# Optimization experiments

Measured on AMD Instinct MI355X. Metric: run time of the kernel, lower is better.

Reference implementation:

```python
import jax, jax.numpy as jnp
import numpy as np

ALPHA = 0.4
EPS = float(np.finfo(np.float32).eps)  # torch.finfo(fp32).eps
BATCH, VOCAB, RANK = 256, 128000, 64


def setup_inputs() -> dict:
    key = jax.random.key(0)
    k1, k2, k3 = jax.random.split(key, 3)
    token_ids = jax.random.randint(k1, (BATCH, 1), 0, VOCAB, dtype=jnp.int64 if jax.config.jax_enable_x64 else jnp.int32)
    logits = jax.random.normal(k2, (BATCH, VOCAB), dtype=jnp.float32)
    W = jax.random.normal(k3, (VOCAB, RANK), dtype=jnp.float32)
    return {"token_ids": token_ids, "logits": logits, "W": W}


def reference(token_ids, logits, W):
    # _rescaled_mint_no_cast (remove_basis=True):
    #   Lp_raw = L @ W @ W.T - L   (low-rank mint, basis removed)
    Lp_raw = (logits @ W) @ W.T - logits  # [B, V]
    # Guarantee max|L'| <= max|L| via global abs-max rescale.
    scale = jnp.max(jnp.abs(logits)) / jnp.maximum(jnp.max(jnp.abs(Lp_raw)), EPS)
    minted = Lp_raw * scale
    # Modes.Lerp: torch.lerp(minted, logits, alpha) = minted + alpha*(logits - minted)
    return minted + ALPHA * (logits - minted)
```

## Files before the change

kernel.cpp:

```cpp
#include <hip/hip_runtime.h>
#include <math.h>

#define ALPHA_F 0.4f
#define FP32_EPS 1.1920928955078125e-7f
#define NB 256
#define NV 128000
#define NR 64

typedef _Float16 half_t;
typedef _Float16 half2_t __attribute__((ext_vector_type(2)));
typedef _Float16 half8 __attribute__((ext_vector_type(8)));
typedef float f32x4 __attribute__((ext_vector_type(4)));


__global__ __launch_bounds__(256) void k0_prep(const float* __restrict__ W,
                                               half_t* __restrict__ WhT,
                                               float* __restrict__ P,
                                               unsigned* __restrict__ maxbits) {
    __shared__ half_t tile[256 * 66];
    const int t  = threadIdx.x;
    const int k0 = blockIdx.x * 256;

    if (blockIdx.x < 64) P[blockIdx.x * 256 + t] = 0.f;
    if (blockIdx.x == 0 && t < 2) maxbits[t] = 0u;

#pragma unroll
    for (int i = 0; i < 16; ++i) {
        const int f  = i * 256 + t;
        const int kr = f >> 4;
        const int n4 = (f & 15) * 4;
        const float4 v = *(const float4*)(W + (size_t)(k0 + kr) * NR + n4);
        half2_t h01 = { (half_t)v.x, (half_t)v.y };
        half2_t h23 = { (half_t)v.z, (half_t)v.w };
        *(half2_t*)&tile[kr * 66 + n4]     = h01;
        *(half2_t*)&tile[kr * 66 + n4 + 2] = h23;
    }
    __syncthreads();

    const int n   = t >> 2;
    const int seg = t & 3;
#pragma unroll
    for (int i = 0; i < 8; ++i) {
        const int kk = (i * 4 + seg) * 8;
        half8 v;
#pragma unroll
        for (int j = 0; j < 8; ++j) v[j] = tile[(kk + j) * 66 + n];
        *(half8*)(WhT + (size_t)n * NV + k0 + kk) = v;
    }
}

__global__ __launch_bounds__(256) void k1_pmm(const float* __restrict__ L,
                                              const half_t* __restrict__ WhT,
                                              float* __restrict__ Ppart,
                                              unsigned* __restrict__ maxbits) {
    const int l  = threadIdx.x & 63;
    const int w  = threadIdx.x >> 6;
    const int q  = l >> 4;
    const int il = l & 15;
    const int k0 = blockIdx.x * 256;

    f32x4 acc[4][4] = {};
    float amax = 0.f;

    for (int ks = 0; ks < 8; ++ks) {
        const int kk = k0 + ks * 32 + q * 8;
        half8 b[4];
#pragma unroll
        for (int nt = 0; nt < 4; ++nt)
            b[nt] = *(const half8*)(WhT + (size_t)(nt * 16 + il) * NV + kk);
#pragma unroll
        for (int mt = 0; mt < 4; ++mt) {
            const float* lp = L + (size_t)(mt * 64 + w * 16 + il) * NV + kk;
            const float4 f0 = *(const float4*)lp;
            const float4 f1 = *(const float4*)(lp + 4);
            amax = fmaxf(amax, fmaxf(fmaxf(fabsf(f0.x), fabsf(f0.y)),
                                     fmaxf(fabsf(f0.z), fabsf(f0.w))));
            amax = fmaxf(amax, fmaxf(fmaxf(fabsf(f1.x), fabsf(f1.y)),
                                     fmaxf(fabsf(f1.z), fabsf(f1.w))));
            half8 a = { (half_t)f0.x, (half_t)f0.y, (half_t)f0.z, (half_t)f0.w,
                        (half_t)f1.x, (half_t)f1.y, (half_t)f1.z, (half_t)f1.w };
#pragma unroll
            for (int nt = 0; nt < 4; ++nt)
                acc[mt][nt] = __builtin_amdgcn_mfma_f32_16x16x32_f16(a, b[nt], acc[mt][nt], 0, 0, 0);
        }
    }

    float* pb = Ppart + (size_t)blockIdx.x * (NB * NR);
#pragma unroll
    for (int mt = 0; mt < 4; ++mt)
#pragma unroll
        for (int nt = 0; nt < 4; ++nt)
#pragma unroll
            for (int i = 0; i < 4; ++i)
                pb[(mt * 64 + w * 16 + q * 4 + i) * NR + nt * 16 + il] = acc[mt][nt][i];

#pragma unroll
    for (int off = 32; off > 0; off >>= 1)
        amax = fmaxf(amax, __shfl_xor(amax, off, 64));
    __shared__ float red[4];
    if (l == 0) red[w] = amax;
    __syncthreads();
    if (threadIdx.x == 0) {
        float m = fmaxf(fmaxf(red[0], red[1]), fmaxf(red[2], red[3]));
        atomicMax(&maxbits[0], __float_as_uint(m));
    }
}

__global__ __launch_bounds__(256) void k1b_reduce(const float* __restrict__ Ppart,
                                                  float* __restrict__ P) {
    const int g = blockIdx.x * 256 + threadIdx.x;
    const float* p = Ppart + (size_t)blockIdx.y * 50 * (NB * NR) + g;
    float s = 0.f;
#pragma unroll 5
    for (int i = 0; i < 50; ++i) s += p[(size_t)i * (NB * NR)];
    atomicAdd(&P[g], s);
}

__global__ __launch_bounds__(256) void k2_max(const float* __restrict__ L,
                                              const float* __restrict__ W,
                                              const float* __restrict__ P,
                                              unsigned* __restrict__ maxbits) {
    const int l  = threadIdx.x & 63;
    const int w  = threadIdx.x >> 6;
    const int q  = l >> 4;
    const int il = l & 15;
    const int m0 = blockIdx.y * 64 + w * 16;

    half8 a[2];
#pragma unroll
    for (int ks = 0; ks < 2; ++ks) {
        const float* pp = P + (m0 + il) * NR + ks * 32 + q * 8;
        const float4 f0 = *(const float4*)pp;
        const float4 f1 = *(const float4*)(pp + 4);
        a[ks] = { (half_t)f0.x, (half_t)f0.y, (half_t)f0.z, (half_t)f0.w,
                  (half_t)f1.x, (half_t)f1.y, (half_t)f1.z, (half_t)f1.w };
    }

    float mx = 0.f;
    for (int it = 0; it < 64; ++it) {
        const int n0 = blockIdx.x * 1024 + it * 16;
        half8 b[2];
#pragma unroll
        for (int ks = 0; ks < 2; ++ks) {
            const float* wp = W + (size_t)(n0 + il) * NR + ks * 32 + q * 8;
            const float4 f0 = *(const float4*)wp;
            const float4 f1 = *(const float4*)(wp + 4);
            b[ks] = { (half_t)f0.x, (half_t)f0.y, (half_t)f0.z, (half_t)f0.w,
                      (half_t)f1.x, (half_t)f1.y, (half_t)f1.z, (half_t)f1.w };
        }
        f32x4 acc = {};
        acc = __builtin_amdgcn_mfma_f32_16x16x32_f16(a[0], b[0], acc, 0, 0, 0);
        acc = __builtin_amdgcn_mfma_f32_16x16x32_f16(a[1], b[1], acc, 0, 0, 0);
        const size_t rowb = (size_t)(m0 + q * 4) * NV + n0 + il;
#pragma unroll
        for (int i = 0; i < 4; ++i) {
            const float lv = L[rowb + (size_t)i * NV];
            mx = fmaxf(mx, fabsf(acc[i] - lv));
        }
    }

#pragma unroll
    for (int off = 32; off > 0; off >>= 1)
        mx = fmaxf(mx, __shfl_xor(mx, off, 64));
    __shared__ float red[4];
    if (l == 0) red[w] = mx;
    __syncthreads();
    if (threadIdx.x == 0) {
        float m = fmaxf(fmaxf(red[0], red[1]), fmaxf(red[2], red[3]));
        atomicMax(&maxbits[1], __float_as_uint(m));
    }
}

__global__ __launch_bounds__(256) void k3_out(const float* __restrict__ L,
                                              const float* __restrict__ W,
                                              const float* __restrict__ P,
                                              const unsigned* __restrict__ maxbits,
                                              float* __restrict__ out) {
    const int l  = threadIdx.x & 63;
    const int w  = threadIdx.x >> 6;
    const int q  = l >> 4;
    const int il = l & 15;
    const int m0 = blockIdx.y * 64 + w * 16;

    const float maxL  = __uint_as_float(maxbits[0]);
    const float maxLp = fmaxf(__uint_as_float(maxbits[1]), FP32_EPS);
    const float scale = maxL / maxLp;
    const float c1 = (1.f - ALPHA_F) * scale;
    const float c0 = ALPHA_F;

    half8 a[2];
#pragma unroll
    for (int ks = 0; ks < 2; ++ks) {
        const float* pp = P + (m0 + il) * NR + ks * 32 + q * 8;
        const float4 f0 = *(const float4*)pp;
        const float4 f1 = *(const float4*)(pp + 4);
        a[ks] = { (half_t)f0.x, (half_t)f0.y, (half_t)f0.z, (half_t)f0.w,
                  (half_t)f1.x, (half_t)f1.y, (half_t)f1.z, (half_t)f1.w };
    }

    for (int it = 0; it < 64; ++it) {
        const int n0 = blockIdx.x * 1024 + it * 16;
        half8 b[2];
#pragma unroll
        for (int ks = 0; ks < 2; ++ks) {
            const float* wp = W + (size_t)(n0 + il) * NR + ks * 32 + q * 8;
            const float4 f0 = *(const float4*)wp;
            const float4 f1 = *(const float4*)(wp + 4);
            b[ks] = { (half_t)f0.x, (half_t)f0.y, (half_t)f0.z, (half_t)f0.w,
                      (half_t)f1.x, (half_t)f1.y, (half_t)f1.z, (half_t)f1.w };
        }
        f32x4 acc = {};
        acc = __builtin_amdgcn_mfma_f32_16x16x32_f16(a[0], b[0], acc, 0, 0, 0);
        acc = __builtin_amdgcn_mfma_f32_16x16x32_f16(a[1], b[1], acc, 0, 0, 0);
        const size_t rowb = (size_t)(m0 + q * 4) * NV + n0 + il;
#pragma unroll
        for (int i = 0; i < 4; ++i) {
            const float lv = L[rowb + (size_t)i * NV];
            out[rowb + (size_t)i * NV] = fmaf(c1, acc[i] - lv, c0 * lv);
        }
    }
}

extern "C" void kernel_launch(void* const* d_in, const int* in_sizes, int n_in,
                              void* d_out, int out_size, void* d_ws, size_t ws_size,
                              hipStream_t stream) {
    const float* L = (const float*)d_in[1];
    const float* W = (const float*)d_in[2];
    float* out = (float*)d_out;

    unsigned* maxbits = (unsigned*)d_ws;
    float*    P       = (float*)((char*)d_ws + 256);

    float*  Ppart = (float*)d_out;
    half_t* WhT   = (half_t*)((char*)d_out + (32u << 20));

    k0_prep  <<<500,          256, 0, stream>>>(W, WhT, P, maxbits);
    k1_pmm   <<<500,          256, 0, stream>>>(L, WhT, Ppart, maxbits);
    k1b_reduce<<<dim3(64,10), 256, 0, stream>>>(Ppart, P);
    k2_max   <<<dim3(125,4),  256, 0, stream>>>(L, W, P, maxbits);
    k3_out   <<<dim3(125,4),  256, 0, stream>>>(L, W, P, maxbits, out);
}
```

Measured before the change: 410.0 us.

## Pre-swizzle W into MFMA fragment layout, cache fp16 logits, coalesce output via LDS

The prep kernel now writes W in per-lane MFMA fragment order for both GEMMs. The first GEMM splits rows across a 4-wide grid dimension and optionally writes an fp16 copy of the logits. The max and output passes become one templated kernel that stages the 64x128 tile in LDS, then reads and writes global memory with coalesced float4 accesses. When the workspace is large enough, those passes read fp16 logits instead of fp32. This halves their logits traffic but adds precision loss to the result and extra writes in the first GEMM.

```diff
diff --git a/kernel.cpp b/kernel.cpp
--- a/kernel.cpp
+++ b/kernel.cpp
@@ -9,15 +9,17 @@
 
 typedef _Float16 half_t;
 typedef _Float16 half2_t __attribute__((ext_vector_type(2)));
+typedef _Float16 half4_t __attribute__((ext_vector_type(4)));
 typedef _Float16 half8 __attribute__((ext_vector_type(8)));
 typedef float f32x4 __attribute__((ext_vector_type(4)));
 
 
 __global__ __launch_bounds__(256) void k0_prep(const float* __restrict__ W,
-                                               half_t* __restrict__ WhT,
+                                               half_t* __restrict__ Wg,
+                                               half_t* __restrict__ Wf,
                                                float* __restrict__ P,
                                                unsigned* __restrict__ maxbits) {
-    __shared__ half_t tile[256 * 66];
+    __shared__ half_t tile[256 * 72];
     const int t  = threadIdx.x;
     const int k0 = blockIdx.x * 256;
 
@@ -32,67 +34,87 @@
         const float4 v = *(const float4*)(W + (size_t)(k0 + kr) * NR + n4);
         half2_t h01 = { (half_t)v.x, (half_t)v.y };
         half2_t h23 = { (half_t)v.z, (half_t)v.w };
-        *(half2_t*)&tile[kr * 66 + n4]     = h01;
-        *(half2_t*)&tile[kr * 66 + n4 + 2] = h23;
+        *(half2_t*)&tile[kr * 72 + n4]     = h01;
+        *(half2_t*)&tile[kr * 72 + n4 + 2] = h23;
     }
     __syncthreads();
 
-    const int n   = t >> 2;
-    const int seg = t & 3;
 #pragma unroll
     for (int i = 0; i < 8; ++i) {
-        const int kk = (i * 4 + seg) * 8;
+        const int idx  = i * 256 + t;
+        const int kk_l = idx >> 8;
+        const int rem  = idx & 255;
+        const int nt   = rem >> 6;
+        const int lane = rem & 63;
+        const int q = lane >> 4, il = lane & 15;
         half8 v;
 #pragma unroll
-        for (int j = 0; j < 8; ++j) v[j] = tile[(kk + j) * 66 + n];
-        *(half8*)(WhT + (size_t)n * NV + k0 + kk) = v;
+        for (int j = 0; j < 8; ++j)
+            v[j] = tile[(kk_l * 32 + q * 8 + j) * 72 + nt * 16 + il];
+        const int kt = blockIdx.x * 8 + kk_l;
+        *(half8*)(Wg + ((size_t)(kt * 4 + nt) * 64 + lane) * 8) = v;
+    }
+
+    if (Wf) {
+#pragma unroll
+        for (int i = 0; i < 8; ++i) {
+            const int idx  = i * 256 + t;
+            const int vt_l = idx >> 7;
+            const int ks   = (idx >> 6) & 1;
+            const int lane = idx & 63;
+            const int q = lane >> 4, il = lane & 15;
+            half8 v = *(const half8*)&tile[(vt_l * 16 + il) * 72 + ks * 32 + q * 8];
+            const int vt = blockIdx.x * 16 + vt_l;
+            *(half8*)(Wf + ((size_t)(vt * 2 + ks) * 64 + lane) * 8) = v;
+        }
     }
 }
 
 __global__ __launch_bounds__(256) void k1_pmm(const float* __restrict__ L,
-                                              const half_t* __restrict__ WhT,
+                                              const half_t* __restrict__ Wg,
                                               float* __restrict__ Ppart,
+                                              half_t* __restrict__ Lh,
                                               unsigned* __restrict__ maxbits) {
     const int l  = threadIdx.x & 63;
     const int w  = threadIdx.x >> 6;
     const int q  = l >> 4;
     const int il = l & 15;
-    const int k0 = blockIdx.x * 256;
-
-    f32x4 acc[4][4] = {};
+    const int chunk = blockIdx.x;
+    const int mq    = blockIdx.y;
+    const int row   = mq * 64 + w * 16 + il;
+    const size_t rowbase = (size_t)row * NV;
+
+    f32x4 acc[4] = {};
     float amax = 0.f;
 
     for (int ks = 0; ks < 8; ++ks) {
-        const int kk = k0 + ks * 32 + q * 8;
+        const int kk = chunk * 256 + ks * 32;
+        const int kt = chunk * 8 + ks;
         half8 b[4];
 #pragma unroll
         for (int nt = 0; nt < 4; ++nt)
-            b[nt] = *(const half8*)(WhT + (size_t)(nt * 16 + il) * NV + kk);
-#pragma unroll
-        for (int mt = 0; mt < 4; ++mt) {
-            const float* lp = L + (size_t)(mt * 64 + w * 16 + il) * NV + kk;
-            const float4 f0 = *(const float4*)lp;
-            const float4 f1 = *(const float4*)(lp + 4);
-            amax = fmaxf(amax, fmaxf(fmaxf(fabsf(f0.x), fabsf(f0.y)),
-                                     fmaxf(fabsf(f0.z), fabsf(f0.w))));
-            amax = fmaxf(amax, fmaxf(fmaxf(fabsf(f1.x), fabsf(f1.y)),
-                                     fmaxf(fabsf(f1.z), fabsf(f1.w))));
-            half8 a = { (half_t)f0.x, (half_t)f0.y, (half_t)f0.z, (half_t)f0.w,
-                        (half_t)f1.x, (half_t)f1.y, (half_t)f1.z, (half_t)f1.w };
-#pragma unroll
-            for (int nt = 0; nt < 4; ++nt)
-                acc[mt][nt] = __builtin_amdgcn_mfma_f32_16x16x32_f16(a, b[nt], acc[mt][nt], 0, 0, 0);
-        }
-    }
-
-    float* pb = Ppart + (size_t)blockIdx.x * (NB * NR);
-#pragma unroll
-    for (int mt = 0; mt < 4; ++mt)
+            b[nt] = *(const half8*)(Wg + ((size_t)(kt * 4 + nt) * 64 + l) * 8);
+        const float* lp = L + rowbase + kk + q * 8;
+        const float4 f0 = *(const float4*)lp;
+        const float4 f1 = *(const float4*)(lp + 4);
+        amax = fmaxf(amax, fmaxf(fmaxf(fabsf(f0.x), fabsf(f0.y)),
+                                 fmaxf(fabsf(f0.z), fabsf(f0.w))));
+        amax = fmaxf(amax, fmaxf(fmaxf(fabsf(f1.x), fabsf(f1.y)),
+                                 fmaxf(fabsf(f1.z), fabsf(f1.w))));
+        half8 a = { (half_t)f0.x, (half_t)f0.y, (half_t)f0.z, (half_t)f0.w,
+                    (half_t)f1.x, (half_t)f1.y, (half_t)f1.z, (half_t)f1.w };
+        if (Lh) *(half8*)(Lh + rowbase + kk + q * 8) = a;
 #pragma unroll
         for (int nt = 0; nt < 4; ++nt)
-#pragma unroll
-            for (int i = 0; i < 4; ++i)
-                pb[(mt * 64 + w * 16 + q * 4 + i) * NR + nt * 16 + il] = acc[mt][nt][i];
+            acc[nt] = __builtin_amdgcn_mfma_f32_16x16x32_f16(a, b[nt], acc[nt], 0, 0, 0);
+    }
+
+    float* pb = Ppart + (size_t)(chunk * 4 + mq) * 4096;
+#pragma unroll
+    for (int nt = 0; nt < 4; ++nt)
+#pragma unroll
+        for (int i = 0; i < 4; ++i)
+            pb[(w * 16 + q * 4 + i) * 64 + nt * 16 + il] = acc[nt][i];
 
 #pragma unroll
     for (int off = 32; off > 0; off >>= 1)
@@ -108,115 +130,114 @@
 
 __global__ __launch_bounds__(256) void k1b_reduce(const float* __restrict__ Ppart,
                                                   float* __restrict__ P) {
-    const int g = blockIdx.x * 256 + threadIdx.x;
-    const float* p = Ppart + (size_t)blockIdx.y * 50 * (NB * NR) + g;
+    const int g  = blockIdx.x * 256 + threadIdx.x;
+    const int M  = g >> 6, n = g & 63;
+    const int mq = M >> 6, r = M & 63;
+    const float* p = Ppart + ((size_t)(blockIdx.y * 100) * 4 + mq) * 4096 + r * 64 + n;
     float s = 0.f;
-#pragma unroll 5
-    for (int i = 0; i < 50; ++i) s += p[(size_t)i * (NB * NR)];
+#pragma unroll 4
+    for (int c = 0; c < 100; ++c) s += p[(size_t)c * 4 * 4096];
     atomicAdd(&P[g], s);
 }
 
-__global__ __launch_bounds__(256) void k2_max(const float* __restrict__ L,
-                                              const float* __restrict__ W,
-                                              const float* __restrict__ P,
-                                              unsigned* __restrict__ maxbits) {
+template <bool FAST, bool IS_OUT>
+__global__ __launch_bounds__(256) void k23(const float* __restrict__ L,
+                                           const half_t* __restrict__ Lh,
+                                           const float* __restrict__ W,
+                                           const half_t* __restrict__ Wf,
+                                           const float* __restrict__ P,
+                                           unsigned* __restrict__ maxbits,
+                                           float* __restrict__ out) {
+    __shared__ float T[64 * 132];
+    __shared__ float red[4];
     const int l  = threadIdx.x & 63;
     const int w  = threadIdx.x >> 6;
     const int q  = l >> 4;
     const int il = l & 15;
-    const int m0 = blockIdx.y * 64 + w * 16;
-
-    half8 a[2];
-#pragma unroll
-    for (int ks = 0; ks < 2; ++ks) {
-        const float* pp = P + (m0 + il) * NR + ks * 32 + q * 8;
-        const float4 f0 = *(const float4*)pp;
-        const float4 f1 = *(const float4*)(pp + 4);
-        a[ks] = { (half_t)f0.x, (half_t)f0.y, (half_t)f0.z, (half_t)f0.w,
-                  (half_t)f1.x, (half_t)f1.y, (half_t)f1.z, (half_t)f1.w };
-    }
-
-    float mx = 0.f;
-    for (int it = 0; it < 64; ++it) {
-        const int n0 = blockIdx.x * 1024 + it * 16;
+    const int nc = blockIdx.x;
+    const int mq = blockIdx.y;
+
+    half8 a[4][2];
+#pragma unroll
+    for (int mt = 0; mt < 4; ++mt)
+#pragma unroll
+        for (int ks = 0; ks < 2; ++ks) {
+            const float* pp = P + (size_t)(mq * 64 + mt * 16 + il) * NR + ks * 32 + q * 8;
+            const float4 f0 = *(const float4*)pp;
+            const float4 f1 = *(const float4*)(pp + 4);
+            a[mt][ks] = { (half_t)f0.x, (half_t)f0.y, (half_t)f0.z, (half_t)f0.w,
+                          (half_t)f1.x, (half_t)f1.y, (half_t)f1.z, (half_t)f1.w };
+        }
+#pragma unroll
+    for (int ntl = 0; ntl < 2; ++ntl) {
+        const int vt = nc * 8 + w * 2 + ntl;
         half8 b[2];
-#pragma unroll
-        for (int ks = 0; ks < 2; ++ks) {
-            const float* wp = W + (size_t)(n0 + il) * NR + ks * 32 + q * 8;
-            const float4 f0 = *(const float4*)wp;
-            const float4 f1 = *(const float4*)(wp + 4);
-            b[ks] = { (half_t)f0.x, (half_t)f0.y, (half_t)f0.z, (half_t)f0.w,
-                      (half_t)f1.x, (half_t)f1.y, (half_t)f1.z, (half_t)f1.w };
-        }
-        f32x4 acc = {};
-        acc = __builtin_amdgcn_mfma_f32_16x16x32_f16(a[0], b[0], acc, 0, 0, 0);
-        acc = __builtin_amdgcn_mfma_f32_16x16x32_f16(a[1], b[1], acc, 0, 0, 0);
-        const size_t rowb = (size_t)(m0 + q * 4) * NV + n0 + il;
-#pragma unroll
-        for (int i = 0; i < 4; ++i) {
-            const float lv = L[rowb + (size_t)i * NV];
-            mx = fmaxf(mx, fabsf(acc[i] - lv));
-        }
-    }
-
-#pragma unroll
-    for (int off = 32; off > 0; off >>= 1)
-        mx = fmaxf(mx, __shfl_xor(mx, off, 64));
-    __shared__ float red[4];
-    if (l == 0) red[w] = mx;
+        if (FAST) {
+#pragma unroll
+            for (int ks = 0; ks < 2; ++ks)
+                b[ks] = *(const half8*)(Wf + ((size_t)(vt * 2 + ks) * 64 + l) * 8);
+        } else {
+#pragma unroll
+            for (int ks = 0; ks < 2; ++ks) {
+                const float* wp = W + (size_t)(vt * 16 + il) * NR + ks * 32 + q * 8;
+                const float4 f0 = *(const float4*)wp;
+                const float4 f1 = *(const float4*)(wp + 4);
+                b[ks] = { (half_t)f0.x, (half_t)f0.y, (half_t)f0.z, (half_t)f0.w,
+                          (half_t)f1.x, (half_t)f1.y, (half_t)f1.z, (half_t)f1.w };
+            }
+        }
+#pragma unroll
+        for (int mt = 0; mt < 4; ++mt) {
+            f32x4 acc = {};
+            acc = __builtin_amdgcn_mfma_f32_16x16x32_f16(a[mt][0], b[0], acc, 0, 0, 0);
+            acc = __builtin_amdgcn_mfma_f32_16x16x32_f16(a[mt][1], b[1], acc, 0, 0, 0);
+#pragma unroll
+            for (int i = 0; i < 4; ++i)
+                T[(mt * 16 + q * 4 + i) * 132 + w * 32 + ntl * 16 + il] = acc[i];
+        }
+    }
     __syncthreads();
-    if (threadIdx.x == 0) {
-        float m = fmaxf(fmaxf(red[0], red[1]), fmaxf(red[2], red[3]));
-        atomicMax(&maxbits[1], __float_as_uint(m));
-    }
-}
-
-__global__ __launch_bounds__(256) void k3_out(const float* __restrict__ L,
-                                              const float* __restrict__ W,
-                                              const float* __restrict__ P,
-                                              const unsigned* __restrict__ maxbits,
-                                              float* __restrict__ out) {
-    const int l  = threadIdx.x & 63;
-    const int w  = threadIdx.x >> 6;
-    const int q  = l >> 4;
-    const int il = l & 15;
-    const int m0 = blockIdx.y * 64 + w * 16;
-
-    const float maxL  = __uint_as_float(maxbits[0]);
-    const float maxLp = fmaxf(__uint_as_float(maxbits[1]), FP32_EPS);
-    const float scale = maxL / maxLp;
-    const float c1 = (1.f - ALPHA_F) * scale;
-    const float c0 = ALPHA_F;
-
-    half8 a[2];
-#pragma unroll
-    for (int ks = 0; ks < 2; ++ks) {
-        const float* pp = P + (m0 + il) * NR + ks * 32 + q * 8;
-        const float4 f0 = *(const float4*)pp;
-        const float4 f1 = *(const float4*)(pp + 4);
-        a[ks] = { (half_t)f0.x, (half_t)f0.y, (half_t)f0.z, (half_t)f0.w,
-                  (half_t)f1.x, (half_t)f1.y, (half_t)f1.z, (half_t)f1.w };
-    }
-
-    for (int it = 0; it < 64; ++it) {
-        const int n0 = blockIdx.x * 1024 + it * 16;
-        half8 b[2];
-#pragma unroll
-        for (int ks = 0; ks < 2; ++ks) {
-            const float* wp = W + (size_t)(n0 + il) * NR + ks * 32 + q * 8;
-            const float4 f0 = *(const float4*)wp;
-            const float4 f1 = *(const float4*)(wp + 4);
-            b[ks] = { (half_t)f0.x, (half_t)f0.y, (half_t)f0.z, (half_t)f0.w,
-                      (half_t)f1.x, (half_t)f1.y, (half_t)f1.z, (half_t)f1.w };
-        }
-        f32x4 acc = {};
-        acc = __builtin_amdgcn_mfma_f32_16x16x32_f16(a[0], b[0], acc, 0, 0, 0);
-        acc = __builtin_amdgcn_mfma_f32_16x16x32_f16(a[1], b[1], acc, 0, 0, 0);
-        const size_t rowb = (size_t)(m0 + q * 4) * NV + n0 + il;
-#pragma unroll
-        for (int i = 0; i < 4; ++i) {
-            const float lv = L[rowb + (size_t)i * NV];
-            out[rowb + (size_t)i * NV] = fmaf(c1, acc[i] - lv, c0 * lv);
+
+    float c1 = 0.f, mx = 0.f;
+    if (IS_OUT) {
+        const float maxL  = __uint_as_float(maxbits[0]);
+        const float maxLp = fmaxf(__uint_as_float(maxbits[1]), FP32_EPS);
+        c1 = (1.f - ALPHA_F) * (maxL / maxLp);
+    }
+#pragma unroll
+    for (int i = 0; i < 8; ++i) {
+        const int e = i * 1024 + threadIdx.x * 4;
+        const int r = e >> 7, c = e & 127;
+        const size_t gaddr = (size_t)(mq * 64 + r) * NV + nc * 128 + c;
+        const float4 tv = *(const float4*)&T[r * 132 + c];
+        float4 lv;
+        if (FAST) {
+            const half4_t lh = *(const half4_t*)(Lh + gaddr);
+            lv = make_float4((float)lh[0], (float)lh[1], (float)lh[2], (float)lh[3]);
+        } else {
+            lv = *(const float4*)(L + gaddr);
+        }
+        if (IS_OUT) {
+            float4 o;
+            o.x = fmaf(c1, tv.x - lv.x, ALPHA_F * lv.x);
+            o.y = fmaf(c1, tv.y - lv.y, ALPHA_F * lv.y);
+            o.z = fmaf(c1, tv.z - lv.z, ALPHA_F * lv.z);
+            o.w = fmaf(c1, tv.w - lv.w, ALPHA_F * lv.w);
+            *(float4*)(out + gaddr) = o;
+        } else {
+            mx = fmaxf(mx, fmaxf(fmaxf(fabsf(tv.x - lv.x), fabsf(tv.y - lv.y)),
+                                 fmaxf(fabsf(tv.z - lv.z), fabsf(tv.w - lv.w))));
+        }
+    }
+    if (!IS_OUT) {
+#pragma unroll
+        for (int off = 32; off > 0; off >>= 1)
+            mx = fmaxf(mx, __shfl_xor(mx, off, 64));
+        if (l == 0) red[w] = mx;
+        __syncthreads();
+        if (threadIdx.x == 0) {
+            float m = fmaxf(fmaxf(red[0], red[1]), fmaxf(red[2], red[3]));
+            atomicMax(&maxbits[1], __float_as_uint(m));
         }
     }
 }
@@ -231,12 +252,29 @@
     unsigned* maxbits = (unsigned*)d_ws;
     float*    P       = (float*)((char*)d_ws + 256);
 
-    float*  Ppart = (float*)d_out;
-    half_t* WhT   = (half_t*)((char*)d_out + (32u << 20));
-
-    k0_prep  <<<500,          256, 0, stream>>>(W, WhT, P, maxbits);
-    k1_pmm   <<<500,          256, 0, stream>>>(L, WhT, Ppart, maxbits);
-    k1b_reduce<<<dim3(64,10), 256, 0, stream>>>(Ppart, P);
-    k2_max   <<<dim3(125,4),  256, 0, stream>>>(L, W, P, maxbits);
-    k3_out   <<<dim3(125,4),  256, 0, stream>>>(L, W, P, maxbits, out);
-}
+    const bool fast = ws_size >= (size_t)140 * 1024 * 1024;
+    float* Ppart; half_t* Wg; half_t* Wf; half_t* Lh;
+    char* ws = (char*)d_ws;
+    if (fast) {
+        Ppart = (float*)(ws + ((size_t)1  << 20));
+        Wg    = (half_t*)(ws + ((size_t)34 << 20));
+        Wf    = (half_t*)(ws + ((size_t)51 << 20));
+        Lh    = (half_t*)(ws + ((size_t)68 << 20));
+    } else {
+        Ppart = (float*)d_out;
+        Wg    = (half_t*)((char*)d_out + ((size_t)33 << 20));
+        Wf    = nullptr;
+        Lh    = nullptr;
+    }
+
+    k0_prep   <<<500,           256, 0, stream>>>(W, Wg, Wf, P, maxbits);
+    k1_pmm    <<<dim3(500, 4),  256, 0, stream>>>(L, Wg, Ppart, Lh, maxbits);
+    k1b_reduce<<<dim3(64, 5),   256, 0, stream>>>(Ppart, P);
+    if (fast) {
+        k23<true,  false><<<dim3(1000, 4), 256, 0, stream>>>(L, Lh, W, Wf, P, maxbits, out);
+        k23<true,  true ><<<dim3(1000, 4), 256, 0, stream>>>(L, Lh, W, Wf, P, maxbits, out);
+    } else {
+        k23<false, false><<<dim3(1000, 4), 256, 0, stream>>>(L, Lh, W, Wf, P, maxbits, out);
+        k23<false, true ><<<dim3(1000, 4), 256, 0, stream>>>(L, Lh, W, Wf, P, maxbits, out);
+    }
+}
```

After: 381.4 us. 1.07x faster.
